# Kernel optimization log

Hardware: AMD Instinct MI355X
Metric: run time of the kernel (lower is better)

Reference implementation:

```python
import jax, jax.numpy as jnp
import numpy as np

R, C, CH, BA = 2048, 1024, 8, 8
EPS = 1e-10


def setup_inputs() -> dict:
    key = jax.random.key(0)
    k1, k2, k3 = jax.random.split(key, 3)
    # kaiming_uniform_ on [R, CH*BA]: fan_in = CH*BA, bound = sqrt(6/fan_in)
    bound = float(np.sqrt(6.0 / (CH * BA)))
    W = jax.random.uniform(k1, (R, CH * BA), jnp.float32, -bound, bound)
    D = (jax.random.uniform(k2, (R, C)) < 0.1).astype(jnp.float32)
    # Gumbel(0,1) noise, replicating the torch quirk: -log(eps - log(u + eps))
    u = jax.random.uniform(k3, (R, CH * BA), jnp.float32)
    g = -jnp.log(EPS - jnp.log(u + EPS))
    return {"W": W, "D": D, "g": g, "i": 100}


def reference(W, D, g, i):
    # temp = 1000 - 999/3999*i is computed in torch but GumbelSoftmax.forward
    # ignores it and always uses temperature=1, so i has no effect on the math.
    P = jax.nn.softmax(W + g, axis=-1).reshape(R, CH, BA)        # [R,CH,BA]
    x = P[:, None, :, :] * D[:, :, None, None]                    # [R,C,CH,BA]

    nnz_ch_ba = jnp.sum(x, axis=(0, 1))                           # [CH,BA]
    max_nnz_ch = jnp.max(nnz_ch_ba, axis=-1)                      # [CH] (torch dim=2 on 2D -> last axis)

    col_ch = 1.0 - jnp.prod(jnp.prod(1.0 - x, axis=0), axis=2)    # [C,CH]
    num_col_ch = jnp.sum(col_ch, axis=0)                          # [CH]
    num_row_ch = jnp.sum(P, axis=(0, 2))                          # [CH]

    col_density_ch = jnp.sum(
        jnp.sum(x, axis=(0, 3)) / num_row_ch / num_col_ch, axis=0)  # [CH]

    tot_ch = max_nnz_ch + num_col_ch + num_row_ch                 # [CH]

    num_row_sel = jnp.sum(
        (jnp.max(P.reshape(R, -1), axis=1) > 0.99).astype(jnp.float32))
    return (P, tot_ch, max_nnz_ch, num_col_ch, num_row_ch,
            nnz_ch_ba, col_density_ch, num_row_sel)
```

## Files before the change

### kernel.cpp

```cpp
#include <hip/hip_runtime.h>
#include <math.h>

#define R 2048
#define C 1024
#define CH 8
#define K 64

#define OFF_P     0
#define OFF_TOT   (R*K)
#define OFF_MAX   (OFF_TOT + 8)
#define OFF_NCOL  (OFF_MAX + 8)
#define OFF_NROW  (OFF_NCOL + 8)
#define OFF_NNZ   (OFF_NROW + 8)
#define OFF_DEN   (OFF_NNZ + 64)
#define OFF_SEL   (OFF_DEN + 8)

#define WS_LQ   0
#define WS_COL  16384
#define WS_NP   24576
#define WS_NR   40960
#define WS_SEL  43008

__global__ __launch_bounds__(512) void k1(
    const float* __restrict__ W, const float* __restrict__ Dm,
    const float* __restrict__ g, float* __restrict__ P,
    float* __restrict__ ws)
{
    const int tid  = threadIdx.x;
    const int lane = tid & 63;
    const int w    = tid >> 6;
    const int row  = blockIdx.x * 8 + w;

    if (tid < 32) ws[WS_COL + blockIdx.x * 32 + tid] = 0.0f;

    float z = W[row * K + lane] + g[row * K + lane];
    float m = z;
    #pragma unroll
    for (int off = 32; off >= 1; off >>= 1)
        m = fmaxf(m, __shfl_xor(m, off, 64));
    float e = __expf(z - m);
    float s = e;
    #pragma unroll
    for (int off = 32; off >= 1; off >>= 1)
        s += __shfl_xor(s, off, 64);
    float p = e * __builtin_amdgcn_rcpf(s);
    P[row * K + lane] = p;

    const float4* Drow = (const float4*)(Dm + (size_t)row * C);
    float ds = 0.0f;
    #pragma unroll
    for (int j = 0; j < 4; ++j) {
        float4 v = Drow[lane + 64 * j];
        ds += (v.x + v.y) + (v.z + v.w);
    }
    #pragma unroll
    for (int off = 32; off >= 1; off >>= 1)
        ds += __shfl_xor(ds, off, 64);

    float om = 1.0f - p, sc = p;
    #pragma unroll
    for (int off = 1; off <= 4; off <<= 1) {
        om *= __shfl_xor(om, off, 64);
        sc += __shfl_xor(sc, off, 64);
    }
    if ((lane & 7) == 0)
        ws[WS_LQ + row * CH + (lane >> 3)] =
            fmaxf(__builtin_amdgcn_logf(om), -1.0e30f);

    float pm = p;
    #pragma unroll
    for (int off = 32; off >= 1; off >>= 1)
        pm = fmaxf(pm, __shfl_xor(pm, off, 64));

    __shared__ float rn[8][64];
    __shared__ float rp[8][8];
    __shared__ float rsel[8];
    rn[w][lane] = p * ds;
    if ((lane & 7) == 0) rp[w][lane >> 3] = sc;
    if (lane == 0) rsel[w] = (pm > 0.99f) ? 1.0f : 0.0f;
    __syncthreads();

    if (tid < 64) {
        float v = rn[0][tid] + rn[1][tid] + rn[2][tid] + rn[3][tid]
                + rn[4][tid] + rn[5][tid] + rn[6][tid] + rn[7][tid];
        ws[WS_NP + blockIdx.x * 64 + tid] = v;
    }
    if (tid < 8) {
        float v = 0.0f;
        #pragma unroll
        for (int ww = 0; ww < 8; ++ww) v += rp[ww][tid];
        ws[WS_NR + blockIdx.x * 8 + tid] = v;
    }
    if (tid == 0) {
        float v = 0.0f;
        #pragma unroll
        for (int ww = 0; ww < 8; ++ww) v += rsel[ww];
        ws[WS_SEL + blockIdx.x] = v;
    }
}

__global__ __launch_bounds__(256) void k2(
    const float* __restrict__ Dm, float* __restrict__ ws)
{
    const int tid = threadIdx.x;
    const int ct  = blockIdx.x & 3;
    const int rc  = blockIdx.x >> 2;
    const int col = ct * 256 + tid;

    float l0=0,l1=0,l2=0,l3=0,l4=0,l5=0,l6=0,l7=0;
    const int r0 = rc * 32;
    #pragma unroll 4
    for (int i = 0; i < 32; ++i) {
        const int r = r0 + i;
        float d = Dm[(size_t)r * C + col];
        const float* lr = ws + WS_LQ + r * CH;
        l0 += d * lr[0]; l1 += d * lr[1]; l2 += d * lr[2]; l3 += d * lr[3];
        l4 += d * lr[4]; l5 += d * lr[5]; l6 += d * lr[6]; l7 += d * lr[7];
    }
    float* ca = ws + WS_COL;
    atomicAdd(&ca[0 * 1024 + col], l0);
    atomicAdd(&ca[1 * 1024 + col], l1);
    atomicAdd(&ca[2 * 1024 + col], l2);
    atomicAdd(&ca[3 * 1024 + col], l3);
    atomicAdd(&ca[4 * 1024 + col], l4);
    atomicAdd(&ca[5 * 1024 + col], l5);
    atomicAdd(&ca[6 * 1024 + col], l6);
    atomicAdd(&ca[7 * 1024 + col], l7);
}

__global__ __launch_bounds__(1024) void k3(const float* __restrict__ ws,
                                           float* __restrict__ out)
{
    const int tid = threadIdx.x;
    __shared__ float red[1024];
    __shared__ float npr[16][64];
    __shared__ float nrr[8][8];
    __shared__ float selr[64];
    __shared__ float nc8[8];

    {
        const int ch = tid >> 7, c0 = tid & 127;
        float ncl = 0.0f;
        #pragma unroll
        for (int j = 0; j < 8; ++j)
            ncl += 1.0f - __builtin_amdgcn_exp2f(
                              ws[WS_COL + ch * 1024 + j * 128 + c0]);
        red[tid] = ncl;
    }
    {
        const int l = tid & 63, grp = tid >> 6;
        float v = 0.0f;
        #pragma unroll
        for (int b = 0; b < 16; ++b)
            v += ws[WS_NP + (grp * 16 + b) * 64 + l];
        npr[grp][l] = v;
    }
    if (tid < 64) {
        const int ch = tid & 7, grp = tid >> 3;
        float v = 0.0f;
        #pragma unroll
        for (int b = 0; b < 32; ++b)
            v += ws[WS_NR + (grp * 32 + b) * CH + ch];
        nrr[grp][ch] = v;
        float sv = 0.0f;
        #pragma unroll
        for (int j = 0; j < 4; ++j)
            sv += ws[WS_SEL + j * 64 + tid];
        selr[tid] = sv;
    }
    __syncthreads();

    #pragma unroll
    for (int off = 64; off >= 1; off >>= 1) {
        if ((tid & 127) < off) red[tid] += red[tid + off];
        __syncthreads();
    }
    if ((tid & 127) == 0) nc8[tid >> 7] = red[tid];
    __syncthreads();

    if (tid < 64) {
        float nnzv = 0.0f;
        #pragma unroll
        for (int g2 = 0; g2 < 16; ++g2) nnzv += npr[g2][tid];
        out[OFF_NNZ + tid] = nnzv;

        float sum = nnzv, mx = nnzv;
        #pragma unroll
        for (int off = 1; off <= 4; off <<= 1) {
            sum += __shfl_xor(sum, off, 64);
            mx = fmaxf(mx, __shfl_xor(mx, off, 64));
        }
        float sv = selr[tid];
        #pragma unroll
        for (int off = 32; off >= 1; off >>= 1)
            sv += __shfl_xor(sv, off, 64);
        if (tid == 0) out[OFF_SEL] = sv;

        if ((tid & 7) == 0) {
            const int ch = tid >> 3;
            float nr = 0.0f;
            #pragma unroll
            for (int g2 = 0; g2 < 8; ++g2) nr += nrr[g2][ch];
            const float nc = nc8[ch];
            out[OFF_TOT  + ch] = mx + nc + nr;
            out[OFF_MAX  + ch] = mx;
            out[OFF_NCOL + ch] = nc;
            out[OFF_NROW + ch] = nr;
            out[OFF_DEN  + ch] = sum / nr / nc;
        }
    }
}

extern "C" void kernel_launch(void* const* d_in, const int* in_sizes, int n_in,
                              void* d_out, int out_size, void* d_ws, size_t ws_size,
                              hipStream_t stream) {
    const float* W = (const float*)d_in[0];
    const float* D = (const float*)d_in[1];
    const float* g = (const float*)d_in[2];
    float* out = (float*)d_out;
    float* ws  = (float*)d_ws;

    k1<<<256, 512, 0, stream>>>(W, D, g, out, ws);
    k2<<<256, 256, 0, stream>>>(D, ws);
    k3<<<1,  1024, 0, stream>>>(ws, out);
}
```

Baseline: 77.13 us.

## Fuse final reduction kernel into k2 via last-block atomic counter

Removes the separate single-block finalize kernel k3 and runs its reductions in whichever k2 block finishes last, detected with a global atomic counter reset in k1. This saves one kernel launch and its launch gap. The price is a threadfence plus counter atomic in every k2 block, and a 256-thread tail reduction that does more serial work per thread than the old 1024-thread one. Column accumulators are read back with atomic adds of zero to make the other blocks' atomics visible.

```diff
diff --git a/kernel.cpp b/kernel.cpp
--- a/kernel.cpp
+++ b/kernel.cpp
@@ -20,6 +20,7 @@
 #define WS_NP   24576
 #define WS_NR   40960
 #define WS_SEL  43008
+#define WS_CNT  43264
 
 __global__ __launch_bounds__(512) void k1(
     const float* __restrict__ W, const float* __restrict__ Dm,
@@ -32,6 +33,7 @@
     const int row  = blockIdx.x * 8 + w;
 
     if (tid < 32) ws[WS_COL + blockIdx.x * 32 + tid] = 0.0f;
+    if (blockIdx.x == 0 && tid == 256) ((unsigned int*)ws)[WS_CNT] = 0u;
 
     float z = W[row * K + lane] + g[row * K + lane];
     float m = z;
@@ -100,7 +102,8 @@
 }
 
 __global__ __launch_bounds__(256) void k2(
-    const float* __restrict__ Dm, float* __restrict__ ws)
+    const float* __restrict__ Dm, float* __restrict__ ws,
+    float* __restrict__ out)
 {
     const int tid = threadIdx.x;
     const int ct  = blockIdx.x & 3;
@@ -126,62 +129,60 @@
     atomicAdd(&ca[5 * 1024 + col], l5);
     atomicAdd(&ca[6 * 1024 + col], l6);
     atomicAdd(&ca[7 * 1024 + col], l7);
-}
-
-__global__ __launch_bounds__(1024) void k3(const float* __restrict__ ws,
-                                           float* __restrict__ out)
-{
-    const int tid = threadIdx.x;
-    __shared__ float red[1024];
-    __shared__ float npr[16][64];
+
+    __threadfence();
+    __syncthreads();
+    __shared__ int is_last;
+    if (tid == 0) {
+        unsigned int old = atomicAdd(&((unsigned int*)ws)[WS_CNT], 1u);
+        is_last = (old == 255u) ? 1 : 0;
+    }
+    __syncthreads();
+    if (!is_last) return;
+
+    __shared__ float red[256];
+    __shared__ float npr[4][64];
     __shared__ float nrr[8][8];
-    __shared__ float selr[64];
     __shared__ float nc8[8];
 
     {
-        const int ch = tid >> 7, c0 = tid & 127;
+        const int ch = tid >> 5, c0 = tid & 31;
         float ncl = 0.0f;
         #pragma unroll
-        for (int j = 0; j < 8; ++j)
-            ncl += 1.0f - __builtin_amdgcn_exp2f(
-                              ws[WS_COL + ch * 1024 + j * 128 + c0]);
+        for (int j = 0; j < 32; ++j) {
+            float v = atomicAdd(&ws[WS_COL + ch * 1024 + j * 32 + c0], 0.0f);
+            ncl += 1.0f - __builtin_amdgcn_exp2f(v);
+        }
         red[tid] = ncl;
     }
     {
         const int l = tid & 63, grp = tid >> 6;
         float v = 0.0f;
         #pragma unroll
-        for (int b = 0; b < 16; ++b)
-            v += ws[WS_NP + (grp * 16 + b) * 64 + l];
+        for (int b = 0; b < 64; ++b)
+            v += ws[WS_NP + (grp * 64 + b) * 64 + l];
         npr[grp][l] = v;
     }
     if (tid < 64) {
-        const int ch = tid & 7, grp = tid >> 3;
+        const int ch = tid & 7, g2 = tid >> 3;
         float v = 0.0f;
         #pragma unroll
         for (int b = 0; b < 32; ++b)
-            v += ws[WS_NR + (grp * 32 + b) * CH + ch];
-        nrr[grp][ch] = v;
-        float sv = 0.0f;
-        #pragma unroll
-        for (int j = 0; j < 4; ++j)
-            sv += ws[WS_SEL + j * 64 + tid];
-        selr[tid] = sv;
-    }
-    __syncthreads();
-
-    #pragma unroll
-    for (int off = 64; off >= 1; off >>= 1) {
-        if ((tid & 127) < off) red[tid] += red[tid + off];
+            v += ws[WS_NR + (g2 * 32 + b) * CH + ch];
+        nrr[g2][ch] = v;
+    }
+    __syncthreads();
+
+    #pragma unroll
+    for (int off = 16; off >= 1; off >>= 1) {
+        if ((tid & 31) < off) red[tid] += red[tid + off];
         __syncthreads();
     }
-    if ((tid & 127) == 0) nc8[tid >> 7] = red[tid];
+    if ((tid & 31) == 0) nc8[tid >> 5] = red[tid];
     __syncthreads();
 
     if (tid < 64) {
-        float nnzv = 0.0f;
-        #pragma unroll
-        for (int g2 = 0; g2 < 16; ++g2) nnzv += npr[g2][tid];
+        float nnzv = npr[0][tid] + npr[1][tid] + npr[2][tid] + npr[3][tid];
         out[OFF_NNZ + tid] = nnzv;
 
         float sum = nnzv, mx = nnzv;
@@ -190,7 +191,9 @@
             sum += __shfl_xor(sum, off, 64);
             mx = fmaxf(mx, __shfl_xor(mx, off, 64));
         }
-        float sv = selr[tid];
+
+        float sv = ws[WS_SEL + tid] + ws[WS_SEL + 64 + tid]
+                 + ws[WS_SEL + 128 + tid] + ws[WS_SEL + 192 + tid];
         #pragma unroll
         for (int off = 32; off >= 1; off >>= 1)
             sv += __shfl_xor(sv, off, 64);
@@ -221,6 +224,5 @@
     float* ws  = (float*)d_ws;
 
     k1<<<256, 512, 0, stream>>>(W, D, g, out, ws);
-    k2<<<256, 256, 0, stream>>>(D, ws);
-    k3<<<1,  1024, 0, stream>>>(ws, out);
+    k2<<<256, 256, 0, stream>>>(D, ws, out);
 }
```

Result: slower. 92.00 us (+19.3%).

## Fuse three kernels into one cooperative kernel with grid-wide syncs

Applied to the files above, without the earlier changes.

Merges the softmax/row-stats kernel, the column log-product accumulation kernel and the final single-block reduction into one cooperative launch separated by grid.sync(). The column stage now uses 512 threads that split rows into two halves, combine partials in shared memory, and load the per-row log values as float4. The aim is to remove two kernel launch gaps. In exchange it adds grid-barrier cost and relies on all 256 blocks of 512 threads being co-resident, which a cooperative launch requires.

```diff
diff --git a/kernel.cpp b/kernel.cpp
--- a/kernel.cpp
+++ b/kernel.cpp
@@ -1,5 +1,8 @@
 #include <hip/hip_runtime.h>
+#include <hip/hip_cooperative_groups.h>
 #include <math.h>
+
+namespace cg = cooperative_groups;
 
 #define R 2048
 #define C 1024
@@ -21,192 +24,200 @@
 #define WS_NR   40960
 #define WS_SEL  43008
 
-__global__ __launch_bounds__(512) void k1(
+__global__ __launch_bounds__(512) void fused(
     const float* __restrict__ W, const float* __restrict__ Dm,
-    const float* __restrict__ g, float* __restrict__ P,
-    float* __restrict__ ws)
+    const float* __restrict__ g, float* __restrict__ ws,
+    float* __restrict__ out)
 {
+    cg::grid_group grid = cg::this_grid();
     const int tid  = threadIdx.x;
     const int lane = tid & 63;
     const int w    = tid >> 6;
-    const int row  = blockIdx.x * 8 + w;
-
-    if (tid < 32) ws[WS_COL + blockIdx.x * 32 + tid] = 0.0f;
-
-    float z = W[row * K + lane] + g[row * K + lane];
-    float m = z;
-    #pragma unroll
-    for (int off = 32; off >= 1; off >>= 1)
-        m = fmaxf(m, __shfl_xor(m, off, 64));
-    float e = __expf(z - m);
-    float s = e;
-    #pragma unroll
-    for (int off = 32; off >= 1; off >>= 1)
-        s += __shfl_xor(s, off, 64);
-    float p = e * __builtin_amdgcn_rcpf(s);
-    P[row * K + lane] = p;
-
-    const float4* Drow = (const float4*)(Dm + (size_t)row * C);
-    float ds = 0.0f;
-    #pragma unroll
-    for (int j = 0; j < 4; ++j) {
-        float4 v = Drow[lane + 64 * j];
-        ds += (v.x + v.y) + (v.z + v.w);
-    }
-    #pragma unroll
-    for (int off = 32; off >= 1; off >>= 1)
-        ds += __shfl_xor(ds, off, 64);
-
-    float om = 1.0f - p, sc = p;
-    #pragma unroll
-    for (int off = 1; off <= 4; off <<= 1) {
-        om *= __shfl_xor(om, off, 64);
-        sc += __shfl_xor(sc, off, 64);
-    }
-    if ((lane & 7) == 0)
-        ws[WS_LQ + row * CH + (lane >> 3)] =
-            fmaxf(__builtin_amdgcn_logf(om), -1.0e30f);
-
-    float pm = p;
-    #pragma unroll
-    for (int off = 32; off >= 1; off >>= 1)
-        pm = fmaxf(pm, __shfl_xor(pm, off, 64));
+    const int b    = blockIdx.x;
 
     __shared__ float rn[8][64];
     __shared__ float rp[8][8];
     __shared__ float rsel[8];
-    rn[w][lane] = p * ds;
-    if ((lane & 7) == 0) rp[w][lane >> 3] = sc;
-    if (lane == 0) rsel[w] = (pm > 0.99f) ? 1.0f : 0.0f;
-    __syncthreads();
-
-    if (tid < 64) {
-        float v = rn[0][tid] + rn[1][tid] + rn[2][tid] + rn[3][tid]
-                + rn[4][tid] + rn[5][tid] + rn[6][tid] + rn[7][tid];
-        ws[WS_NP + blockIdx.x * 64 + tid] = v;
-    }
-    if (tid < 8) {
-        float v = 0.0f;
-        #pragma unroll
-        for (int ww = 0; ww < 8; ++ww) v += rp[ww][tid];
-        ws[WS_NR + blockIdx.x * 8 + tid] = v;
-    }
-    if (tid == 0) {
-        float v = 0.0f;
-        #pragma unroll
-        for (int ww = 0; ww < 8; ++ww) v += rsel[ww];
-        ws[WS_SEL + blockIdx.x] = v;
-    }
-}
-
-__global__ __launch_bounds__(256) void k2(
-    const float* __restrict__ Dm, float* __restrict__ ws)
-{
-    const int tid = threadIdx.x;
-    const int ct  = blockIdx.x & 3;
-    const int rc  = blockIdx.x >> 2;
-    const int col = ct * 256 + tid;
-
-    float l0=0,l1=0,l2=0,l3=0,l4=0,l5=0,l6=0,l7=0;
-    const int r0 = rc * 32;
-    #pragma unroll 4
-    for (int i = 0; i < 32; ++i) {
-        const int r = r0 + i;
-        float d = Dm[(size_t)r * C + col];
-        const float* lr = ws + WS_LQ + r * CH;
-        l0 += d * lr[0]; l1 += d * lr[1]; l2 += d * lr[2]; l3 += d * lr[3];
-        l4 += d * lr[4]; l5 += d * lr[5]; l6 += d * lr[6]; l7 += d * lr[7];
-    }
-    float* ca = ws + WS_COL;
-    atomicAdd(&ca[0 * 1024 + col], l0);
-    atomicAdd(&ca[1 * 1024 + col], l1);
-    atomicAdd(&ca[2 * 1024 + col], l2);
-    atomicAdd(&ca[3 * 1024 + col], l3);
-    atomicAdd(&ca[4 * 1024 + col], l4);
-    atomicAdd(&ca[5 * 1024 + col], l5);
-    atomicAdd(&ca[6 * 1024 + col], l6);
-    atomicAdd(&ca[7 * 1024 + col], l7);
-}
-
-__global__ __launch_bounds__(1024) void k3(const float* __restrict__ ws,
-                                           float* __restrict__ out)
-{
-    const int tid = threadIdx.x;
-    __shared__ float red[1024];
-    __shared__ float npr[16][64];
+    __shared__ float part[2][256][8];
+    __shared__ float red[512];
+    __shared__ float npr[8][64];
     __shared__ float nrr[8][8];
     __shared__ float selr[64];
     __shared__ float nc8[8];
 
     {
-        const int ch = tid >> 7, c0 = tid & 127;
-        float ncl = 0.0f;
-        #pragma unroll
-        for (int j = 0; j < 8; ++j)
-            ncl += 1.0f - __builtin_amdgcn_exp2f(
-                              ws[WS_COL + ch * 1024 + j * 128 + c0]);
-        red[tid] = ncl;
+        const int row = b * 8 + w;
+        if (tid < 32) ws[WS_COL + b * 32 + tid] = 0.0f;
+
+        float z = W[row * K + lane] + g[row * K + lane];
+        float m = z;
+        #pragma unroll
+        for (int off = 32; off >= 1; off >>= 1)
+            m = fmaxf(m, __shfl_xor(m, off, 64));
+        float e = __expf(z - m);
+        float s = e;
+        #pragma unroll
+        for (int off = 32; off >= 1; off >>= 1)
+            s += __shfl_xor(s, off, 64);
+        float p = e * __builtin_amdgcn_rcpf(s);
+        out[OFF_P + row * K + lane] = p;
+
+        const float4* Drow = (const float4*)(Dm + (size_t)row * C);
+        float ds = 0.0f;
+        #pragma unroll
+        for (int j = 0; j < 4; ++j) {
+            float4 v = Drow[lane + 64 * j];
+            ds += (v.x + v.y) + (v.z + v.w);
+        }
+        #pragma unroll
+        for (int off = 32; off >= 1; off >>= 1)
+            ds += __shfl_xor(ds, off, 64);
+
+        float om = 1.0f - p, sc = p;
+        #pragma unroll
+        for (int off = 1; off <= 4; off <<= 1) {
+            om *= __shfl_xor(om, off, 64);
+            sc += __shfl_xor(sc, off, 64);
+        }
+        if ((lane & 7) == 0)
+            ws[WS_LQ + row * CH + (lane >> 3)] =
+                fmaxf(__builtin_amdgcn_logf(om), -1.0e30f);
+
+        float pm = p;
+        #pragma unroll
+        for (int off = 32; off >= 1; off >>= 1)
+            pm = fmaxf(pm, __shfl_xor(pm, off, 64));
+
+        rn[w][lane] = p * ds;
+        if ((lane & 7) == 0) rp[w][lane >> 3] = sc;
+        if (lane == 0) rsel[w] = (pm > 0.99f) ? 1.0f : 0.0f;
+        __syncthreads();
+
+        if (tid < 64) {
+            float v = rn[0][tid] + rn[1][tid] + rn[2][tid] + rn[3][tid]
+                    + rn[4][tid] + rn[5][tid] + rn[6][tid] + rn[7][tid];
+            ws[WS_NP + b * 64 + tid] = v;
+        }
+        if (tid < 8) {
+            float v = 0.0f;
+            #pragma unroll
+            for (int ww = 0; ww < 8; ++ww) v += rp[ww][tid];
+            ws[WS_NR + b * 8 + tid] = v;
+        }
+        if (tid == 0) {
+            float v = 0.0f;
+            #pragma unroll
+            for (int ww = 0; ww < 8; ++ww) v += rsel[ww];
+            ws[WS_SEL + b] = v;
+        }
     }
+    grid.sync();
+
     {
-        const int l = tid & 63, grp = tid >> 6;
-        float v = 0.0f;
-        #pragma unroll
-        for (int b = 0; b < 16; ++b)
-            v += ws[WS_NP + (grp * 16 + b) * 64 + l];
-        npr[grp][l] = v;
+        const int ct  = b & 3;
+        const int rc  = b >> 2;
+        const int s   = tid >> 8;
+        const int c   = tid & 255;
+        const int col = ct * 256 + c;
+
+        float l0=0,l1=0,l2=0,l3=0,l4=0,l5=0,l6=0,l7=0;
+        const int r0 = rc * 32 + s * 16;
+        #pragma unroll 4
+        for (int i = 0; i < 16; ++i) {
+            const int r = r0 + i;
+            float d = Dm[(size_t)r * C + col];
+            float4 qa = *(const float4*)(ws + WS_LQ + r * CH);
+            float4 qb = *(const float4*)(ws + WS_LQ + r * CH + 4);
+            l0 += d * qa.x; l1 += d * qa.y; l2 += d * qa.z; l3 += d * qa.w;
+            l4 += d * qb.x; l5 += d * qb.y; l6 += d * qb.z; l7 += d * qb.w;
+        }
+        part[s][c][0] = l0; part[s][c][1] = l1;
+        part[s][c][2] = l2; part[s][c][3] = l3;
+        part[s][c][4] = l4; part[s][c][5] = l5;
+        part[s][c][6] = l6; part[s][c][7] = l7;
+        __syncthreads();
+
+        #pragma unroll
+        for (int ps = 0; ps < 4; ++ps) {
+            const int flat = ps * 512 + tid;
+            const int cc = flat >> 3, ch = flat & 7;
+            float v = part[0][cc][ch] + part[1][cc][ch];
+            atomicAdd(&ws[WS_COL + ch * 1024 + ct * 256 + cc], v);
+        }
     }
-    if (tid < 64) {
-        const int ch = tid & 7, grp = tid >> 3;
-        float v = 0.0f;
-        #pragma unroll
-        for (int b = 0; b < 32; ++b)
-            v += ws[WS_NR + (grp * 32 + b) * CH + ch];
-        nrr[grp][ch] = v;
-        float sv = 0.0f;
-        #pragma unroll
-        for (int j = 0; j < 4; ++j)
-            sv += ws[WS_SEL + j * 64 + tid];
-        selr[tid] = sv;
-    }
-    __syncthreads();
-
-    #pragma unroll
-    for (int off = 64; off >= 1; off >>= 1) {
-        if ((tid & 127) < off) red[tid] += red[tid + off];
-        __syncthreads();
-    }
-    if ((tid & 127) == 0) nc8[tid >> 7] = red[tid];
-    __syncthreads();
-
-    if (tid < 64) {
-        float nnzv = 0.0f;
-        #pragma unroll
-        for (int g2 = 0; g2 < 16; ++g2) nnzv += npr[g2][tid];
-        out[OFF_NNZ + tid] = nnzv;
-
-        float sum = nnzv, mx = nnzv;
-        #pragma unroll
-        for (int off = 1; off <= 4; off <<= 1) {
-            sum += __shfl_xor(sum, off, 64);
-            mx = fmaxf(mx, __shfl_xor(mx, off, 64));
-        }
-        float sv = selr[tid];
-        #pragma unroll
-        for (int off = 32; off >= 1; off >>= 1)
-            sv += __shfl_xor(sv, off, 64);
-        if (tid == 0) out[OFF_SEL] = sv;
-
-        if ((tid & 7) == 0) {
-            const int ch = tid >> 3;
-            float nr = 0.0f;
-            #pragma unroll
-            for (int g2 = 0; g2 < 8; ++g2) nr += nrr[g2][ch];
-            const float nc = nc8[ch];
-            out[OFF_TOT  + ch] = mx + nc + nr;
-            out[OFF_MAX  + ch] = mx;
-            out[OFF_NCOL + ch] = nc;
-            out[OFF_NROW + ch] = nr;
-            out[OFF_DEN  + ch] = sum / nr / nc;
+    grid.sync();
+
+    if (b != 0) return;
+    {
+        {
+            const int ch = tid >> 6, c0 = tid & 63;
+            float ncl = 0.0f;
+            #pragma unroll
+            for (int j = 0; j < 16; ++j)
+                ncl += 1.0f - __builtin_amdgcn_exp2f(
+                                  ws[WS_COL + ch * 1024 + j * 64 + c0]);
+            red[tid] = ncl;
+        }
+        {
+            const int l = tid & 63, grp = tid >> 6;
+            float v = 0.0f;
+            #pragma unroll
+            for (int bb = 0; bb < 32; ++bb)
+                v += ws[WS_NP + (grp * 32 + bb) * 64 + l];
+            npr[grp][l] = v;
+        }
+        if (tid < 64) {
+            const int ch = tid & 7, g2 = tid >> 3;
+            float v = 0.0f;
+            #pragma unroll
+            for (int bb = 0; bb < 32; ++bb)
+                v += ws[WS_NR + (g2 * 32 + bb) * CH + ch];
+            nrr[g2][ch] = v;
+            float sv = 0.0f;
+            #pragma unroll
+            for (int j = 0; j < 4; ++j)
+                sv += ws[WS_SEL + j * 64 + tid];
+            selr[tid] = sv;
+        }
+        __syncthreads();
+
+        #pragma unroll
+        for (int off = 32; off >= 1; off >>= 1) {
+            if ((tid & 63) < off) red[tid] += red[tid + off];
+            __syncthreads();
+        }
+        if ((tid & 63) == 0) nc8[tid >> 6] = red[tid];
+        __syncthreads();
+
+        if (tid < 64) {
+            float nnzv = npr[0][tid] + npr[1][tid] + npr[2][tid] + npr[3][tid]
+                       + npr[4][tid] + npr[5][tid] + npr[6][tid] + npr[7][tid];
+            out[OFF_NNZ + tid] = nnzv;
+
+            float sum = nnzv, mx = nnzv;
+            #pragma unroll
+            for (int off = 1; off <= 4; off <<= 1) {
+                sum += __shfl_xor(sum, off, 64);
+                mx = fmaxf(mx, __shfl_xor(mx, off, 64));
+            }
+            float sv = selr[tid];
+            #pragma unroll
+            for (int off = 32; off >= 1; off >>= 1)
+                sv += __shfl_xor(sv, off, 64);
+            if (tid == 0) out[OFF_SEL] = sv;
+
+            if ((tid & 7) == 0) {
+                const int ch = tid >> 3;
+                float nr = 0.0f;
+                #pragma unroll
+                for (int g2 = 0; g2 < 8; ++g2) nr += nrr[g2][ch];
+                const float nc = nc8[ch];
+                out[OFF_TOT  + ch] = mx + nc + nr;
+                out[OFF_MAX  + ch] = mx;
+                out[OFF_NCOL + ch] = nc;
+                out[OFF_NROW + ch] = nr;
+                out[OFF_DEN  + ch] = sum / nr / nc;
+            }
         }
     }
 }
@@ -220,7 +231,7 @@
     float* out = (float*)d_out;
     float* ws  = (float*)d_ws;
 
-    k1<<<256, 512, 0, stream>>>(W, D, g, out, ws);
-    k2<<<256, 256, 0, stream>>>(D, ws);
-    k3<<<1,  1024, 0, stream>>>(ws, out);
+    void* args[] = { (void*)&W, (void*)&D, (void*)&g, (void*)&ws, (void*)&out };
+    hipLaunchCooperativeKernel((void*)fused, dim3(256), dim3(512),
+                               args, 0, stream);
 }
```

Result: slower. 137.8 us (+78.7%).
